# Kernel optimization log

Measured on AMD Instinct MI355X. Metric: run time of the kernel, lower is better.

Reference implementation:

```python
import jax, jax.numpy as jnp
import numpy as np

B, T, D = 4, 2048, 2048
DV = 1024
T_IMG, N_LAT = 8, 64
H, DH = 16, 64
INNER = H * DH
EPS = 1e-5


def setup_inputs() -> dict:
    key = jax.random.key(0)
    ks = jax.random.split(key, 8)
    x = jax.random.normal(ks[0], (B, T, D), dtype=jnp.float32)
    media = jax.random.normal(ks[1], (B, T_IMG, N_LAT, DV), dtype=jnp.float32)
    # exactly T_IMG media tokens per sequence, evenly spaced
    pos = (jnp.arange(T_IMG) + 1) * (T // (T_IMG + 1))
    media_locations = jnp.zeros((B, T), dtype=bool).at[:, pos].set(True)
    gamma = jnp.ones((D,), dtype=jnp.float32)
    beta = jnp.zeros((D,), dtype=jnp.float32)
    Wq = jax.random.normal(ks[2], (D, INNER), dtype=jnp.float32) * (D ** -0.5)
    Wkv = jax.random.normal(ks[3], (DV, 2 * INNER), dtype=jnp.float32) * (DV ** -0.5)
    Wout = jax.random.normal(ks[4], (INNER, D), dtype=jnp.float32) * (INNER ** -0.5)
    return {"x": x, "media": media, "media_locations": media_locations,
            "gamma": gamma, "beta": beta, "Wq": Wq, "Wkv": Wkv, "Wout": Wout}


def reference(x, media, media_locations, gamma, beta, Wq, Wkv, Wout):
    scale = DH ** -0.5
    # LayerNorm
    mu = jnp.mean(x, axis=-1, keepdims=True)
    var = jnp.mean(jnp.square(x - mu), axis=-1, keepdims=True)
    xn = (x - mu) * jax.lax.rsqrt(var + EPS) * gamma + beta
    q = xn @ Wq                                   # (B,T,INNER)
    media_f = media.reshape(B, T_IMG * N_LAT, DV)  # (B,J,DV)
    kv = media_f @ Wkv                             # (B,J,2*INNER)
    k, v = jnp.split(kv, 2, axis=-1)
    q = q.reshape(B, T, H, DH).transpose(0, 2, 1, 3) * scale   # (B,H,T,DH)
    k = k.reshape(B, -1, H, DH).transpose(0, 2, 1, 3)          # (B,H,J,DH)
    v = v.reshape(B, -1, H, DH).transpose(0, 2, 1, 3)
    sim = jnp.einsum('bhid,bhjd->bhij', q, k)      # (B,H,T,J)
    # media-location mask: text attends only to its immediately preceding media
    text_time = jnp.cumsum(media_locations.astype(jnp.int32), axis=-1)  # (B,T)
    media_time = jnp.arange(T_IMG, dtype=jnp.int32) + 1                 # (J_img,)
    media_time = jnp.repeat(media_time, N_LAT)                          # (J,)
    mask = text_time[:, None, :, None] == media_time[None, None, None, :]  # (B,1,T,J)
    neg = -jnp.finfo(sim.dtype).max
    sim = jnp.where(mask, sim, neg)
    sim = sim - jax.lax.stop_gradient(jnp.max(sim, axis=-1, keepdims=True))
    attn = jax.nn.softmax(sim, axis=-1)
    # zero attention for text positions with no preceding media
    no_media = (text_time == 0)[:, None, :, None]  # (B,1,T,1)
    attn = jnp.where(no_media, 0.0, attn)
    out = jnp.einsum('bhij,bhjd->bhid', attn, v)   # (B,H,T,DH)
    out = out.transpose(0, 2, 1, 3).reshape(B, T, INNER)
    return out @ Wout
```

## Files before the change

kernel.cpp:

```cpp
#include <hip/hip_runtime.h>
#include <hip/hip_bf16.h>

#define B_ 4
#define T_ 2048
#define D_ 2048
#define DV_ 1024
#define TIMG_ 8
#define NLAT_ 64
#define H_ 16
#define DH_ 64
#define INNER_ 1024
#define J_ (TIMG_ * NLAT_)

using f32x4 = __attribute__((ext_vector_type(4))) float;
using bf16x8 = __attribute__((ext_vector_type(8))) short;
using bf16x4 = __attribute__((ext_vector_type(4))) short;

__device__ __forceinline__ unsigned short f2bf(float f) {
  union { float f; unsigned int u; } c{f};
  unsigned int r = c.u + 0x7FFFu + ((c.u >> 16) & 1u);
  return (unsigned short)(r >> 16);
}

__device__ __forceinline__ void stage16(const unsigned short* g, unsigned short* l) {
  __builtin_amdgcn_global_load_lds(
      (const __attribute__((address_space(1))) unsigned int*)g,
      (__attribute__((address_space(3))) unsigned int*)l, 16, 0, 0);
}

__global__ __launch_bounds__(256) void scan_kernel(const void* __restrict__ locs,
                                                   int* __restrict__ img_idx) {
  __shared__ int sm[256];
  const int tid = threadIdx.x;
  const int b = blockIdx.x;
  const unsigned char* u8 = (const unsigned char*)locs;
  int cnt = 0;
  for (int i = tid; i < B_ * T_; i += 256) cnt += (u8[i] != 0) ? 1 : 0;
  sm[tid] = cnt;
  __syncthreads();
  for (int off = 128; off > 0; off >>= 1) {
    if (tid < off) sm[tid] += sm[tid + off];
    __syncthreads();
  }
  const bool u8mode = (sm[0] == B_ * TIMG_);
  __syncthreads();

  const int base = b * T_ + tid * 8;
  const int* i32 = (const int*)locs;
  int v[8];
  int ts = 0;
#pragma unroll
  for (int j = 0; j < 8; ++j) {
    v[j] = u8mode ? (u8[base + j] != 0 ? 1 : 0) : (i32[base + j] != 0 ? 1 : 0);
    ts += v[j];
  }
  sm[tid] = ts;
  __syncthreads();
  for (int off = 1; off < 256; off <<= 1) {
    int add = (tid >= off) ? sm[tid - off] : 0;
    __syncthreads();
    sm[tid] += add;
    __syncthreads();
  }
  int acc = sm[tid] - ts;
#pragma unroll
  for (int j = 0; j < 8; ++j) {
    acc += v[j];
    img_idx[base + j] = acc - 1;
  }
}

__global__ __launch_bounds__(256) void ln_kernel(const float* __restrict__ x,
                                                 const float* __restrict__ g,
                                                 const float* __restrict__ bta,
                                                 unsigned short* __restrict__ xn) {
  const int row = blockIdx.x;
  const int tid = threadIdx.x;
  const float4* xr = (const float4*)(x + (size_t)row * D_);
  float4 v0 = xr[tid];
  float4 v1 = xr[tid + 256];
  float s = v0.x + v0.y + v0.z + v0.w + v1.x + v1.y + v1.z + v1.w;
  float sq = v0.x * v0.x + v0.y * v0.y + v0.z * v0.z + v0.w * v0.w +
             v1.x * v1.x + v1.y * v1.y + v1.z * v1.z + v1.w * v1.w;
#pragma unroll
  for (int off = 32; off > 0; off >>= 1) {
    s += __shfl_xor(s, off);
    sq += __shfl_xor(sq, off);
  }
  __shared__ float ls[4], lq[4];
  const int lane = tid & 63, wave = tid >> 6;
  if (lane == 0) { ls[wave] = s; lq[wave] = sq; }
  __syncthreads();
  s = ls[0] + ls[1] + ls[2] + ls[3];
  sq = lq[0] + lq[1] + lq[2] + lq[3];
  const float mu = s * (1.0f / D_);
  const float rstd = rsqrtf(sq * (1.0f / D_) - mu * mu + 1e-5f);
  const float4* gv4 = (const float4*)g;
  const float4* bv4 = (const float4*)bta;
  ushort4* o4 = (ushort4*)(xn + (size_t)row * D_);
#pragma unroll
  for (int i = 0; i < 2; ++i) {
    const int idx = tid + i * 256;
    float4 vv = i == 0 ? v0 : v1;
    float4 gv = gv4[idx];
    float4 bv = bv4[idx];
    ushort4 o = make_ushort4(f2bf((vv.x - mu) * rstd * gv.x + bv.x),
                             f2bf((vv.y - mu) * rstd * gv.y + bv.y),
                             f2bf((vv.z - mu) * rstd * gv.z + bv.z),
                             f2bf((vv.w - mu) * rstd * gv.w + bv.w));
    o4[idx] = o;
  }
}

__global__ void tcast(const float* __restrict__ in, unsigned short* __restrict__ out,
                      int R, int C, float scale) {
  __shared__ float tile[32][33];
  const int bc = blockIdx.x * 32;
  const int br = blockIdx.y * 32;
  const int tx = threadIdx.x, ty = threadIdx.y;
#pragma unroll
  for (int i = ty; i < 32; i += 8)
    tile[i][tx] = in[(size_t)(br + i) * C + bc + tx];
  __syncthreads();
#pragma unroll
  for (int i = ty; i < 32; i += 8)
    out[(size_t)(bc + i) * R + br + tx] = f2bf(tile[tx][i] * scale);
}

__global__ void cast_bf16(const float* __restrict__ in, unsigned short* __restrict__ out,
                          int n4) {
  int i = blockIdx.x * blockDim.x + threadIdx.x;
  if (i >= n4) return;
  float4 v = ((const float4*)in)[i];
  ((ushort4*)out)[i] = make_ushort4(f2bf(v.x), f2bf(v.y), f2bf(v.z), f2bf(v.w));
}

__global__ void vtrans(const unsigned short* __restrict__ kvb, unsigned short* __restrict__ vt) {
  __shared__ unsigned short tile[32][33];
  const int jt = blockIdx.x * 32;
  const int dt = blockIdx.y * 32;
  const int b = blockIdx.z;
  const int tx = threadIdx.x, ty = threadIdx.y;
#pragma unroll
  for (int i = ty; i < 32; i += 8)
    tile[i][tx] = kvb[(size_t)(b * J_ + jt + i) * (2 * INNER_) + INNER_ + dt + tx];
  __syncthreads();
#pragma unroll
  for (int i = ty; i < 32; i += 8)
    vt[(size_t)(b * INNER_ + dt + i) * J_ + jt + tx] = tile[tx][i];
}

template <bool BF16OUT>
__global__ __launch_bounds__(512, 2) void gemm_8ph(const unsigned short* __restrict__ Ag,
                                                   const unsigned short* __restrict__ Bg,
                                                   void* __restrict__ Cv,
                                                   int M, int N, int K) {
  __shared__ __align__(16) unsigned short lds[2][24576];
  const int tid = threadIdx.x;
  const int lane = tid & 63;
  const int wave = tid >> 6;
  const int l15 = lane & 15;
  const int lg8 = (lane >> 4) << 3;
  const int wr64 = (wave >> 2) << 6;
  const int wc16 = (wave & 3) << 4;

  const int nwg = gridDim.x;
  int wg = ((int)blockIdx.x & 7) * (nwg >> 3) + ((int)blockIdx.x >> 3);
  const int gridM = M >> 7;
  const long row0 = (long)(wg % gridM) << 7;
  const long col0 = (long)(wg / gridM) << 8;

  auto stageA = [&](int buf, int kt, int r) {
    const int i = r * 512 + tid;
    const int row = i >> 3;
    const int c = (i & 7) ^ (row & 7);
    stage16(Ag + (size_t)(row0 + row) * K + kt + c * 8, &lds[buf][i * 8]);
  };
  auto stageB = [&](int buf, int kt, int r) {
    const int i = r * 512 + tid;
    const int row = i >> 3;
    const int c = (i & 7) ^ (row & 7);
    stage16(Bg + (size_t)(col0 + row) * K + kt + c * 8, &lds[buf][8192 + i * 8]);
  };

  const int NT = K >> 6;
  stageA(0, 0, 0); stageA(0, 0, 1);
  stageB(0, 0, 0); stageB(0, 0, 1); stageB(0, 0, 2); stageB(0, 0, 3);
  stageA(1, 64, 0); stageA(1, 64, 1);
  stageB(1, 64, 0); stageB(1, 64, 1); stageB(1, 64, 2); stageB(1, 64, 3);
  asm volatile("s_waitcnt vmcnt(6)" ::: "memory");
  asm volatile("s_barrier" ::: "memory");

  f32x4 acc[4][4] = {};
  int cur = 0;
  for (int t = 0; t < NT; ++t, cur ^= 1) {
    const unsigned short* Ab = &lds[cur][0];
    const unsigned short* Bb = &lds[cur][8192];
    bf16x8 af[4][2], bfr[4][2];
#pragma unroll
    for (int m = 0; m < 4; ++m)
#pragma unroll
      for (int kk = 0; kk < 2; ++kk) {
        const int row = wr64 + m * 16 + l15;
        af[m][kk] = *(const bf16x8*)(Ab + row * 64 + ((kk * 32 + lg8) ^ ((row & 7) << 3)));
      }
#pragma unroll
    for (int n = 0; n < 2; ++n)
#pragma unroll
      for (int kk = 0; kk < 2; ++kk) {
        const int brow = n * 64 + wc16 + l15;
        bfr[n][kk] = *(const bf16x8*)(Bb + brow * 64 + ((kk * 32 + lg8) ^ ((brow & 7) << 3)));
      }
    if (t >= 1 && t + 1 < NT) {
      stageB(cur ^ 1, (t + 1) << 6, 2); stageB(cur ^ 1, (t + 1) << 6, 3);
    }
    asm volatile("s_waitcnt vmcnt(6)" ::: "memory");
    asm volatile("s_barrier" ::: "memory");
    asm volatile("s_waitcnt lgkmcnt(0)" ::: "memory");
    __builtin_amdgcn_s_setprio(1);
#pragma unroll
    for (int m = 0; m < 4; ++m)
#pragma unroll
      for (int n = 0; n < 2; ++n)
#pragma unroll
        for (int kk = 0; kk < 2; ++kk)
          acc[m][n] = __builtin_amdgcn_mfma_f32_16x16x32_bf16(af[m][kk], bfr[n][kk], acc[m][n], 0, 0, 0);
    __builtin_amdgcn_s_setprio(0);
    asm volatile("s_barrier" ::: "memory");
#pragma unroll
    for (int n = 2; n < 4; ++n)
#pragma unroll
      for (int kk = 0; kk < 2; ++kk) {
        const int brow = n * 64 + wc16 + l15;
        bfr[n][kk] = *(const bf16x8*)(Bb + brow * 64 + ((kk * 32 + lg8) ^ ((brow & 7) << 3)));
      }
    if (t + 2 < NT) {
      stageA(cur, (t + 2) << 6, 0); stageA(cur, (t + 2) << 6, 1);
      stageB(cur, (t + 2) << 6, 0); stageB(cur, (t + 2) << 6, 1);
    }
    asm volatile("s_waitcnt vmcnt(6)" ::: "memory");
    asm volatile("s_barrier" ::: "memory");
    asm volatile("s_waitcnt lgkmcnt(0)" ::: "memory");
    __builtin_amdgcn_s_setprio(1);
#pragma unroll
    for (int m = 0; m < 4; ++m)
#pragma unroll
      for (int n = 2; n < 4; ++n)
#pragma unroll
        for (int kk = 0; kk < 2; ++kk)
          acc[m][n] = __builtin_amdgcn_mfma_f32_16x16x32_bf16(af[m][kk], bfr[n][kk], acc[m][n], 0, 0, 0);
    __builtin_amdgcn_s_setprio(0);
    asm volatile("s_barrier" ::: "memory");
  }

  const int cr = (lane >> 4) << 2;
#pragma unroll
  for (int m = 0; m < 4; ++m)
#pragma unroll
    for (int n = 0; n < 4; ++n)
#pragma unroll
      for (int j = 0; j < 4; ++j) {
        const size_t idx = (row0 + wr64 + m * 16 + cr + j) * (size_t)N + col0 + n * 64 + wc16 + l15;
        if constexpr (BF16OUT)
          ((unsigned short*)Cv)[idx] = f2bf(acc[m][n][j]);
        else
          ((float*)Cv)[idx] = acc[m][n][j];
      }
}

__global__ __launch_bounds__(256) void attn2_kernel(
    const unsigned short* __restrict__ qb,
    const unsigned short* __restrict__ kvb,
    const unsigned short* __restrict__ vt,
    const int* __restrict__ img_idx,
    unsigned short* __restrict__ attn_out) {
  __shared__ unsigned short Pl[4][64 * 72];
  const int tid = threadIdx.x;
  const int lane = tid & 63;
  const int w = tid >> 6;
  int bid = blockIdx.x;
  const int hg = bid & 3; bid >>= 2;
  const int tile = bid & 31; bid >>= 5;
  const int b = bid;
  const int t0 = tile * 64;
  const int h = hg * 4 + w;
  const int l15 = lane & 15;
  const int lg = lane >> 4;

  const int* ii = img_idx + b * T_ + t0;
  int myimg = ii[lane];
  int tmin = myimg, tmax = myimg;
#pragma unroll
  for (int off = 1; off < 64; off <<= 1) {
    tmin = min(tmin, __shfl_xor(tmin, off));
    tmax = max(tmax, __shfl_xor(tmax, off));
  }
  unsigned short* op = attn_out + (size_t)(b * T_ + t0) * INNER_ + h * DH_;
  if (tmin < 0) {
    for (int r = 0; r < 64; ++r)
      if (ii[r] < 0) op[(size_t)r * INNER_ + lane] = 0;
  }
  if (tmax < 0) return;

  bf16x8 qa[4][2];
  const unsigned short* qrow = qb + (size_t)(b * T_ + t0) * INNER_ + h * DH_;
#pragma unroll
  for (int m = 0; m < 4; ++m)
#pragma unroll
    for (int kk = 0; kk < 2; ++kk)
      qa[m][kk] = *(const bf16x8*)(qrow + (size_t)(l15 + m * 16) * INNER_ + kk * 32 + lg * 8);

  unsigned short* pw = Pl[w];
  for (int img = max(tmin, 0); img <= tmax; ++img) {
    const unsigned short* Kb = kvb + (size_t)(b * J_ + img * NLAT_) * (2 * INNER_) + h * DH_;
    f32x4 acc[4][4] = {};
#pragma unroll
    for (int kk = 0; kk < 2; ++kk) {
      bf16x8 bfr[4];
#pragma unroll
      for (int n = 0; n < 4; ++n)
        bfr[n] = *(const bf16x8*)(Kb + (size_t)(l15 + n * 16) * (2 * INNER_) + kk * 32 + lg * 8);
#pragma unroll
      for (int m = 0; m < 4; ++m)
#pragma unroll
        for (int n = 0; n < 4; ++n)
          acc[m][n] = __builtin_amdgcn_mfma_f32_16x16x32_bf16(qa[m][kk], bfr[n], acc[m][n], 0, 0, 0);
    }
#pragma unroll
    for (int m = 0; m < 4; ++m) {
#pragma unroll
      for (int j = 0; j < 4; ++j) {
        float mx = fmaxf(fmaxf(acc[m][0][j], acc[m][1][j]), fmaxf(acc[m][2][j], acc[m][3][j]));
#pragma unroll
        for (int off = 1; off < 16; off <<= 1) mx = fmaxf(mx, __shfl_xor(mx, off));
        float sum = 0.f;
#pragma unroll
        for (int n = 0; n < 4; ++n) {
          float e = __expf(acc[m][n][j] - mx);
          acc[m][n][j] = e;
          sum += e;
        }
#pragma unroll
        for (int off = 1; off < 16; off <<= 1) sum += __shfl_xor(sum, off);
        const float ri = 1.0f / sum;
        const int row = m * 16 + lg * 4 + j;
#pragma unroll
        for (int n = 0; n < 4; ++n)
          pw[row * 72 + n * 16 + l15] = f2bf(acc[m][n][j] * ri);
      }
    }
    const unsigned short* Vb = vt + (size_t)(b * INNER_ + h * DH_) * J_ + img * NLAT_;
    f32x4 oacc[4][4] = {};
#pragma unroll
    for (int kk = 0; kk < 2; ++kk) {
      bf16x8 pa[4], bfr[4];
#pragma unroll
      for (int m = 0; m < 4; ++m) {
        bf16x4 lo = *(const bf16x4*)(pw + (m * 16 + l15) * 72 + kk * 32 + lg * 8);
        bf16x4 hi = *(const bf16x4*)(pw + (m * 16 + l15) * 72 + kk * 32 + lg * 8 + 4);
        bf16x8 v;
#pragma unroll
        for (int e = 0; e < 4; ++e) { v[e] = lo[e]; v[e + 4] = hi[e]; }
        pa[m] = v;
      }
#pragma unroll
      for (int n = 0; n < 4; ++n)
        bfr[n] = *(const bf16x8*)(Vb + (size_t)(l15 + n * 16) * J_ + kk * 32 + lg * 8);
#pragma unroll
      for (int m = 0; m < 4; ++m)
#pragma unroll
        for (int n = 0; n < 4; ++n)
          oacc[m][n] = __builtin_amdgcn_mfma_f32_16x16x32_bf16(pa[m], bfr[n], oacc[m][n], 0, 0, 0);
    }
#pragma unroll
    for (int m = 0; m < 4; ++m)
#pragma unroll
      for (int j = 0; j < 4; ++j) {
        const int row = m * 16 + lg * 4 + j;
        if (ii[row] == img) {
#pragma unroll
          for (int n = 0; n < 4; ++n)
            op[(size_t)row * INNER_ + n * 16 + l15] = f2bf(oacc[m][n][j]);
        }
      }
  }
}

extern "C" void kernel_launch(void* const* d_in, const int* in_sizes, int n_in,
                              void* d_out, int out_size, void* d_ws, size_t ws_size,
                              hipStream_t stream) {
  const float* x = (const float*)d_in[0];
  const float* media = (const float*)d_in[1];
  const void* mloc = d_in[2];
  const float* gamma = (const float*)d_in[3];
  const float* beta = (const float*)d_in[4];
  const float* Wq = (const float*)d_in[5];
  const float* Wkv = (const float*)d_in[6];
  const float* Wout = (const float*)d_in[7];
  float* out = (float*)d_out;

  char* ws = (char*)d_ws;
  unsigned short* xn = (unsigned short*)(ws);
  unsigned short* wqt = (unsigned short*)(ws + 33554432);
  unsigned short* wkvt = (unsigned short*)(ws + 37748736);
  unsigned short* woutt = (unsigned short*)(ws + 41943040);
  unsigned short* medb = (unsigned short*)(ws + 46137344);
  unsigned short* qb = (unsigned short*)(ws + 50331648);
  unsigned short* kvb = (unsigned short*)(ws + 67108864);
  unsigned short* vt = (unsigned short*)(ws + 75497472);
  int* img_idx = (int*)(ws + 79691776);
  unsigned short* attn_out = xn;

  scan_kernel<<<B_, 256, 0, stream>>>(mloc, img_idx);
  ln_kernel<<<B_ * T_, 256, 0, stream>>>(x, gamma, beta, xn);
  tcast<<<dim3(INNER_ / 32, D_ / 32), dim3(32, 8), 0, stream>>>(Wq, wqt, D_, INNER_, 0.125f);
  tcast<<<dim3(2 * INNER_ / 32, DV_ / 32), dim3(32, 8), 0, stream>>>(Wkv, wkvt, DV_, 2 * INNER_, 1.0f);
  tcast<<<dim3(D_ / 32, INNER_ / 32), dim3(32, 8), 0, stream>>>(Wout, woutt, INNER_, D_, 1.0f);
  cast_bf16<<<(B_ * J_ * DV_ / 4 + 255) / 256, 256, 0, stream>>>(media, medb, B_ * J_ * DV_ / 4);
  gemm_8ph<true><<<(B_ * T_ / 128) * (INNER_ / 256), 512, 0, stream>>>(xn, wqt, qb, B_ * T_, INNER_, D_);
  gemm_8ph<true><<<(B_ * J_ / 128) * (2 * INNER_ / 256), 512, 0, stream>>>(medb, wkvt, kvb, B_ * J_, 2 * INNER_, DV_);
  vtrans<<<dim3(J_ / 32, INNER_ / 32, B_), dim3(32, 8), 0, stream>>>(kvb, vt);
  attn2_kernel<<<B_ * (T_ / 64) * 4, 256, 0, stream>>>(qb, kvb, vt, img_idx, attn_out);
  gemm_8ph<false><<<(B_ * T_ / 128) * (D_ / 256), 512, 0, stream>>>(attn_out, woutt, out, B_ * T_, D_, INNER_);
}
```

Baseline: 173.9 us.

## Use 256x256-tile pipelined GEMM kernel for output projection

Adds a new GEMM kernel with 256x256 output tiles, double-buffered swizzled LDS staging interleaved with MFMA phases, and an XCD-aware block remap, then uses it for the final Wout projection instead of the 128x256 kernel. Larger tiles raise arithmetic intensity and cut global reads of A and B. In exchange the kernel uses 128KB of LDS and many accumulator registers per thread, which limits occupancy, and grid size falls to 256 blocks.

```diff
diff --git a/kernel.cpp b/kernel.cpp
--- a/kernel.cpp
+++ b/kernel.cpp
@@ -261,6 +261,151 @@
 #pragma unroll
       for (int j = 0; j < 4; ++j) {
         const size_t idx = (row0 + wr64 + m * 16 + cr + j) * (size_t)N + col0 + n * 64 + wc16 + l15;
+        if constexpr (BF16OUT)
+          ((unsigned short*)Cv)[idx] = f2bf(acc[m][n][j]);
+        else
+          ((float*)Cv)[idx] = acc[m][n][j];
+      }
+}
+
+template <bool BF16OUT>
+__global__ __launch_bounds__(512, 2) void gemm256(const unsigned short* __restrict__ Ag,
+                                                  const unsigned short* __restrict__ Bg,
+                                                  void* __restrict__ Cv,
+                                                  int M, int N, int K) {
+  __shared__ __align__(16) unsigned short lds[2][32768];
+  const int tid = threadIdx.x;
+  const int lane = tid & 63;
+  const int wave = tid >> 6;
+  const int l15 = lane & 15;
+  const int lg8 = (lane >> 4) << 3;
+  const int wm = (wave >> 2) << 7;
+  const int wn = (wave & 3) << 6;
+
+  const int nwg = gridDim.x;
+  int wg = ((int)blockIdx.x & 7) * (nwg >> 3) + ((int)blockIdx.x >> 3);
+  const int gridM = M >> 8;
+  const long row0 = (long)(wg % gridM) << 8;
+  const long col0 = (long)(wg / gridM) << 8;
+
+  auto stA = [&](int buf, int kt, int r) {
+    const int i = r * 512 + tid;
+    const int row = i >> 3;
+    const int c = (i & 7) ^ (row & 7);
+    stage16(Ag + (size_t)(row0 + row) * K + kt + c * 8, &lds[buf][i * 8]);
+  };
+  auto stB = [&](int buf, int kt, int r) {
+    const int i = r * 512 + tid;
+    const int row = i >> 3;
+    const int c = (i & 7) ^ (row & 7);
+    stage16(Bg + (size_t)(col0 + row) * K + kt + c * 8, &lds[buf][16384 + i * 8]);
+  };
+
+  const int NT = K >> 6;
+  stB(0, 0, 0); stB(0, 0, 1); stB(0, 0, 2); stB(0, 0, 3);
+  stA(0, 0, 0); stA(0, 0, 1); stA(0, 0, 2); stA(0, 0, 3);
+  stB(1, 64, 0); stB(1, 64, 1); stB(1, 64, 2); stB(1, 64, 3);
+  asm volatile("s_waitcnt vmcnt(4)" ::: "memory");
+  asm volatile("s_barrier" ::: "memory");
+
+  f32x4 acc[8][4] = {};
+  int cur = 0;
+  for (int t = 0; t < NT; ++t, cur ^= 1) {
+    const unsigned short* Ab = &lds[cur][0];
+    const unsigned short* Bb = &lds[cur][16384];
+    bf16x8 af[4][2], bfr[4][2];
+    const int ktn = (t + 1) << 6;
+    const int ktn2 = (t + 2) << 6;
+#pragma unroll
+    for (int m = 0; m < 4; ++m)
+#pragma unroll
+      for (int kk = 0; kk < 2; ++kk) {
+        const int row = wm + m * 16 + l15;
+        af[m][kk] = *(const bf16x8*)(Ab + row * 64 + ((kk * 32 + lg8) ^ ((row & 7) << 3)));
+      }
+#pragma unroll
+    for (int n = 0; n < 2; ++n)
+#pragma unroll
+      for (int kk = 0; kk < 2; ++kk) {
+        const int brow = wn + n * 16 + l15;
+        bfr[n][kk] = *(const bf16x8*)(Bb + brow * 64 + ((kk * 32 + lg8) ^ ((brow & 7) << 3)));
+      }
+    if (t + 1 < NT) { stA(cur ^ 1, ktn, 0); stA(cur ^ 1, ktn, 1); }
+    asm volatile("s_barrier" ::: "memory");
+    asm volatile("s_waitcnt lgkmcnt(0)" ::: "memory");
+    __builtin_amdgcn_s_setprio(1);
+#pragma unroll
+    for (int m = 0; m < 4; ++m)
+#pragma unroll
+      for (int n = 0; n < 2; ++n)
+#pragma unroll
+        for (int kk = 0; kk < 2; ++kk)
+          acc[m][n] = __builtin_amdgcn_mfma_f32_16x16x32_bf16(af[m][kk], bfr[n][kk], acc[m][n], 0, 0, 0);
+    __builtin_amdgcn_s_setprio(0);
+    asm volatile("s_barrier" ::: "memory");
+#pragma unroll
+    for (int n = 2; n < 4; ++n)
+#pragma unroll
+      for (int kk = 0; kk < 2; ++kk) {
+        const int brow = wn + n * 16 + l15;
+        bfr[n][kk] = *(const bf16x8*)(Bb + brow * 64 + ((kk * 32 + lg8) ^ ((brow & 7) << 3)));
+      }
+    if (t + 1 < NT) { stA(cur ^ 1, ktn, 2); stA(cur ^ 1, ktn, 3); }
+    asm volatile("s_barrier" ::: "memory");
+    asm volatile("s_waitcnt lgkmcnt(0)" ::: "memory");
+    __builtin_amdgcn_s_setprio(1);
+#pragma unroll
+    for (int m = 0; m < 4; ++m)
+#pragma unroll
+      for (int n = 2; n < 4; ++n)
+#pragma unroll
+        for (int kk = 0; kk < 2; ++kk)
+          acc[m][n] = __builtin_amdgcn_mfma_f32_16x16x32_bf16(af[m][kk], bfr[n][kk], acc[m][n], 0, 0, 0);
+    __builtin_amdgcn_s_setprio(0);
+    asm volatile("s_barrier" ::: "memory");
+#pragma unroll
+    for (int m = 0; m < 4; ++m)
+#pragma unroll
+      for (int kk = 0; kk < 2; ++kk) {
+        const int row = wm + (m + 4) * 16 + l15;
+        af[m][kk] = *(const bf16x8*)(Ab + row * 64 + ((kk * 32 + lg8) ^ ((row & 7) << 3)));
+      }
+    if (t + 2 < NT) { stB(cur, ktn2, 0); stB(cur, ktn2, 1); }
+    asm volatile("s_barrier" ::: "memory");
+    asm volatile("s_waitcnt lgkmcnt(0)" ::: "memory");
+    __builtin_amdgcn_s_setprio(1);
+#pragma unroll
+    for (int m = 0; m < 4; ++m)
+#pragma unroll
+      for (int n = 0; n < 2; ++n)
+#pragma unroll
+        for (int kk = 0; kk < 2; ++kk)
+          acc[m + 4][n] = __builtin_amdgcn_mfma_f32_16x16x32_bf16(af[m][kk], bfr[n][kk], acc[m + 4][n], 0, 0, 0);
+    __builtin_amdgcn_s_setprio(0);
+    asm volatile("s_barrier" ::: "memory");
+    if (t + 2 < NT) { stB(cur, ktn2, 2); stB(cur, ktn2, 3); }
+    asm volatile("s_waitcnt vmcnt(4)" ::: "memory");
+    asm volatile("s_barrier" ::: "memory");
+    __builtin_amdgcn_s_setprio(1);
+#pragma unroll
+    for (int m = 0; m < 4; ++m)
+#pragma unroll
+      for (int n = 2; n < 4; ++n)
+#pragma unroll
+        for (int kk = 0; kk < 2; ++kk)
+          acc[m + 4][n] = __builtin_amdgcn_mfma_f32_16x16x32_bf16(af[m][kk], bfr[n][kk], acc[m + 4][n], 0, 0, 0);
+    __builtin_amdgcn_s_setprio(0);
+    asm volatile("s_barrier" ::: "memory");
+  }
+
+  const int cr = (lane >> 4) << 2;
+#pragma unroll
+  for (int m = 0; m < 8; ++m)
+#pragma unroll
+    for (int n = 0; n < 4; ++n)
+#pragma unroll
+      for (int j = 0; j < 4; ++j) {
+        const size_t idx = (row0 + wm + m * 16 + cr + j) * (size_t)N + col0 + wn + n * 16 + l15;
         if constexpr (BF16OUT)
           ((unsigned short*)Cv)[idx] = f2bf(acc[m][n][j]);
         else
@@ -421,5 +566,5 @@
   gemm_8ph<true><<<(B_ * J_ / 128) * (2 * INNER_ / 256), 512, 0, stream>>>(medb, wkvt, kvb, B_ * J_, 2 * INNER_, DV_);
   vtrans<<<dim3(J_ / 32, INNER_ / 32, B_), dim3(32, 8), 0, stream>>>(kvb, vt);
   attn2_kernel<<<B_ * (T_ / 64) * 4, 256, 0, stream>>>(qb, kvb, vt, img_idx, attn_out);
-  gemm_8ph<false><<<(B_ * T_ / 128) * (D_ / 256), 512, 0, stream>>>(attn_out, woutt, out, B_ * T_, D_, INNER_);
-}
+  gemm256<false><<<(B_ * T_ / 256) * (D_ / 256), 512, 0, stream>>>(attn_out, woutt, out, B_ * T_, D_, INNER_);
+}
```

After: 164.6 us. -5.3%, faster.
